# Kernel tuning notes

Measured on AMD Instinct MI355X. Metric: run time of the kernel, lower is better.

## Reference

```python
import jax, jax.numpy as jnp
import numpy as np

N_NODES = 50000
N_EDGES = 800000
N_LABEL_EDGES = 200000
IN_CH = 256
HID = 64
OUT_CH = 64


def gcn_conv(x, W, b, edge_index, n_nodes):
    """PyG GCNConv: symmetric-normalized aggregation with self-loops.
    out[col] = sum_row norm(row,col) * (x @ W)[row] + b
    """
    xw = x @ W  # [N, out]
    loops = jnp.arange(n_nodes, dtype=edge_index.dtype)
    row = jnp.concatenate([edge_index[0], loops])  # source
    col = jnp.concatenate([edge_index[1], loops])  # target
    deg = jax.ops.segment_sum(jnp.ones_like(col, dtype=xw.dtype), col, num_segments=n_nodes)
    dis = jnp.where(deg > 0, jax.lax.rsqrt(deg), 0.0)
    norm = dis[row] * dis[col]  # [E+N]
    out = jax.ops.segment_sum(xw[row] * norm[:, None], col, num_segments=n_nodes)
    return out + b


def setup_inputs() -> dict:
    key = jax.random.key(0)
    k0, k1, k2, k3, k4 = jax.random.split(key, 5)
    x = jax.random.normal(k0, (N_NODES, IN_CH), dtype=jnp.float32)
    edge_index = jax.random.randint(k1, (2, N_EDGES), 0, N_NODES, dtype=jnp.int32)
    edge_label_index = jax.random.randint(k2, (2, N_LABEL_EDGES), 0, N_NODES, dtype=jnp.int32)
    W1 = jax.random.normal(k3, (IN_CH, HID), dtype=jnp.float32) * (1.0 / np.sqrt(IN_CH))
    b1 = jnp.zeros((HID,), dtype=jnp.float32)
    W2 = jax.random.normal(k4, (HID, OUT_CH), dtype=jnp.float32) * (1.0 / np.sqrt(HID))
    b2 = jnp.zeros((OUT_CH,), dtype=jnp.float32)
    return {"x": x, "edge_index": edge_index, "edge_label_index": edge_label_index,
            "W1": W1, "b1": b1, "W2": W2, "b2": b2}


def reference(x, edge_index, edge_label_index, W1, b1, W2, b2):
    n = x.shape[0]
    # encode: two GCNConv layers with ReLU between
    h = jax.nn.relu(gcn_conv(x, W1, b1, edge_index, n))
    z = gcn_conv(h, W2, b2, edge_index, n)
    # decode: gather node pairs, elementwise multiply, sum over features
    src, dst = edge_label_index[0], edge_label_index[1]
    return jnp.sum(z[src] * z[dst], axis=1)  # [N_LABEL_EDGES]
```

## Files before the change

kernel.cpp:

```cpp
#include <hip/hip_runtime.h>
#include <hip/hip_bf16.h>


constexpr int NC = 256;
constexpr int NBPAD = 256;
constexpr int BSHIFT = 8;

__device__ __forceinline__ unsigned short f2bf(float f) {
    unsigned u = __float_as_uint(f);
    return (unsigned short)((u + 0x7FFF + ((u >> 16) & 1)) >> 16);
}
__device__ __forceinline__ float bf2f(unsigned short h) {
    return __uint_as_float(((unsigned)h) << 16);
}
__device__ __forceinline__ float4 bf4_to_f4(ushort4 u) {
    return make_float4(bf2f(u.x), bf2f(u.y), bf2f(u.z), bf2f(u.w));
}

__global__ __launch_bounds__(256) void hist_kernel(const int* __restrict__ col,
                                                   int* __restrict__ hist, int E, int CE) {
    __shared__ int hl[NBPAD];
    const int t = threadIdx.x, c = blockIdx.x;
    hl[t] = 0;
    __syncthreads();
    const int s = c * CE, e = min(E, s + CE);
    for (int i = s + t; i < e; i += 256) atomicAdd(&hl[col[i] >> BSHIFT], 1);
    __syncthreads();
    hist[t * NC + c] = hl[t];
}

__global__ __launch_bounds__(256) void bsum_kernel(const int* __restrict__ hist,
                                                   int* __restrict__ bsums) {
    __shared__ int red[256];
    const int t = threadIdx.x, b = blockIdx.x;
    red[t] = hist[b * NC + t];
    __syncthreads();
    for (int off = 128; off > 0; off >>= 1) {
        if (t < off) red[t] += red[t + off];
        __syncthreads();
    }
    if (t == 0) bsums[b] = red[0];
}

__global__ __launch_bounds__(256) void bscan_kernel(int* __restrict__ bsums) {
    __shared__ int sc[256];
    const int t = threadIdx.x;
    const int v = bsums[t];
    sc[t] = v;
    __syncthreads();
    for (int off = 1; off < 256; off <<= 1) {
        int u = (t >= off) ? sc[t - off] : 0;
        __syncthreads();
        sc[t] += u;
        __syncthreads();
    }
    bsums[t] = sc[t] - v;
}

__global__ __launch_bounds__(256) void rowscan_kernel(int* __restrict__ hist,
                                                      const int* __restrict__ bsums) {
    __shared__ int sc[256];
    const int t = threadIdx.x, b = blockIdx.x;
    const int v = hist[b * NC + t];
    sc[t] = v;
    __syncthreads();
    for (int off = 1; off < 256; off <<= 1) {
        int u = (t >= off) ? sc[t - off] : 0;
        __syncthreads();
        sc[t] += u;
        __syncthreads();
    }
    hist[b * NC + t] = sc[t] - v + bsums[b];
}

__global__ __launch_bounds__(256) void reorder_kernel(const int* __restrict__ row,
                                                      const int* __restrict__ col,
                                                      const int* __restrict__ hist,
                                                      int2* __restrict__ part, int E, int CE) {
    __shared__ int cur[NBPAD];
    const int t = threadIdx.x, c = blockIdx.x;
    cur[t] = hist[t * NC + c];
    __syncthreads();
    const int s = c * CE, e = min(E, s + CE);
    for (int i = s + t; i < e; i += 256) {
        const int r = row[i], cl = col[i];
        const int p = atomicAdd(&cur[cl >> BSHIFT], 1);
        part[p] = make_int2(r, cl);
    }
}

__global__ __launch_bounds__(256) void bucket_csr_kernel(const int2* __restrict__ part,
                                                         const int* __restrict__ hist,
                                                         int* __restrict__ csr,
                                                         int* __restrict__ offs,
                                                         float* __restrict__ dis,
                                                         int N, int E, int nbk) {
    __shared__ int cnt[256];
    __shared__ int sc[256];
    const int t = threadIdx.x, b = blockIdx.x;
    const int base = b << BSHIFT;
    const int bstart = hist[b * NC];
    const int bend = (b + 1 < NBPAD) ? hist[(b + 1) * NC] : E;
    const int m = bend - bstart;
    cnt[t] = 0;
    __syncthreads();
    for (int i = t; i < m; i += 256) atomicAdd(&cnt[part[bstart + i].y - base], 1);
    __syncthreads();
    const int v = cnt[t];
    sc[t] = v;
    __syncthreads();
    for (int off = 1; off < 256; off <<= 1) {
        int u = (t >= off) ? sc[t - off] : 0;
        __syncthreads();
        sc[t] += u;
        __syncthreads();
    }
    const int excl = sc[t] - v;
    const int node = base + t;
    if (node < N) {
        offs[node] = bstart + excl;
        dis[node] = rsqrtf((float)(v + 1));
    }
    sc[t] = excl;
    __syncthreads();
    for (int i = t; i < m; i += 256) {
        const int2 ec = part[bstart + i];
        const int p = atomicAdd(&sc[ec.y - base], 1);
        csr[bstart + p] = ec.x;
    }
    if (b == nbk - 1 && t == 0) offs[N] = E;
}

template <int K>
__global__ __launch_bounds__(256) void gemm_tile(const float* __restrict__ X,
                                                 const float* __restrict__ W,
                                                 const float* __restrict__ rowscale,
                                                 unsigned short* __restrict__ Y, int nrows) {
    __shared__ float sX[64 * 64];
    __shared__ float sW[64 * 64];
    const int tid = threadIdx.x;
    const int tx = tid & 15;
    const int ty = tid >> 4;
    const int rowbase = blockIdx.x * 64;

    float acc[16];
    #pragma unroll
    for (int i = 0; i < 16; ++i) acc[i] = 0.f;

    const int lr = tid & 63;
    const int lq = tid >> 6;
    int grow = rowbase + lr;
    if (grow >= nrows) grow = nrows - 1;
    const float* xrow = X + (long)grow * K;

    for (int kc = 0; kc < K; kc += 64) {
        if (kc) __syncthreads();
        #pragma unroll
        for (int i = 0; i < 4; ++i) {
            const int o = tid * 4 + i * 1024;
            *(float4*)&sW[o] = *(const float4*)&W[(long)kc * 64 + o];
        }
        #pragma unroll
        for (int t = 0; t < 4; ++t) {
            const int k = lq * 16 + t * 4;
            const float4 v = *(const float4*)&xrow[kc + k];
            sX[(k + 0) * 64 + lr] = v.x;
            sX[(k + 1) * 64 + lr] = v.y;
            sX[(k + 2) * 64 + lr] = v.z;
            sX[(k + 3) * 64 + lr] = v.w;
        }
        __syncthreads();
        #pragma unroll 4
        for (int k = 0; k < 64; ++k) {
            const float4 xv = *(const float4*)&sX[k * 64 + ty * 4];
            const float4 wv = *(const float4*)&sW[k * 64 + tx * 4];
            acc[0]  = fmaf(xv.x, wv.x, acc[0]);
            acc[1]  = fmaf(xv.x, wv.y, acc[1]);
            acc[2]  = fmaf(xv.x, wv.z, acc[2]);
            acc[3]  = fmaf(xv.x, wv.w, acc[3]);
            acc[4]  = fmaf(xv.y, wv.x, acc[4]);
            acc[5]  = fmaf(xv.y, wv.y, acc[5]);
            acc[6]  = fmaf(xv.y, wv.z, acc[6]);
            acc[7]  = fmaf(xv.y, wv.w, acc[7]);
            acc[8]  = fmaf(xv.z, wv.x, acc[8]);
            acc[9]  = fmaf(xv.z, wv.y, acc[9]);
            acc[10] = fmaf(xv.z, wv.z, acc[10]);
            acc[11] = fmaf(xv.z, wv.w, acc[11]);
            acc[12] = fmaf(xv.w, wv.x, acc[12]);
            acc[13] = fmaf(xv.w, wv.y, acc[13]);
            acc[14] = fmaf(xv.w, wv.z, acc[14]);
            acc[15] = fmaf(xv.w, wv.w, acc[15]);
        }
    }

    #pragma unroll
    for (int i = 0; i < 4; ++i) {
        const int orow = rowbase + ty * 4 + i;
        if (orow < nrows) {
            const float d = rowscale[orow];
            ushort4 ov;
            ov.x = f2bf(d * acc[i * 4 + 0]);
            ov.y = f2bf(d * acc[i * 4 + 1]);
            ov.z = f2bf(d * acc[i * 4 + 2]);
            ov.w = f2bf(d * acc[i * 4 + 3]);
            *(ushort4*)&Y[(long)orow * 64 + tx * 4] = ov;
        }
    }
}

template <bool RELU, bool OUT_BF16>
__global__ __launch_bounds__(256) void agg_kernel(const unsigned short* __restrict__ xs,
                                                  const int* __restrict__ csr,
                                                  const int* __restrict__ offs,
                                                  const float* __restrict__ dis,
                                                  const float* __restrict__ bias,
                                                  void* __restrict__ out, int n) {
    __shared__ int sidx[4][64];
    const int wv = threadIdx.x >> 6;
    const int lane = threadIdx.x & 63;
    const int grp = lane >> 4;
    const int fl = lane & 15;
    const int i = blockIdx.x * 4 + wv;
    if (i >= n) return;
    float4 acc = make_float4(0.f, 0.f, 0.f, 0.f);
    if (grp == 0)
        acc = bf4_to_f4(*(const ushort4*)&xs[(long)i * 64 + fl * 4]);
    const int s = offs[i];
    const int e = offs[i + 1];
    for (int jb = s; jb < e; jb += 64) {
        const int nb = min(64, e - jb);
        if (lane < nb) sidx[wv][lane] = csr[jb + lane];
        int u = grp;
        for (; u + 4 < nb; u += 8) {
            const int r0 = sidx[wv][u];
            const int r1 = sidx[wv][u + 4];
            const float4 v0 = bf4_to_f4(*(const ushort4*)&xs[(long)r0 * 64 + fl * 4]);
            const float4 v1 = bf4_to_f4(*(const ushort4*)&xs[(long)r1 * 64 + fl * 4]);
            acc.x += v0.x + v1.x; acc.y += v0.y + v1.y;
            acc.z += v0.z + v1.z; acc.w += v0.w + v1.w;
        }
        for (; u < nb; u += 4) {
            const int r0 = sidx[wv][u];
            const float4 v0 = bf4_to_f4(*(const ushort4*)&xs[(long)r0 * 64 + fl * 4]);
            acc.x += v0.x; acc.y += v0.y; acc.z += v0.z; acc.w += v0.w;
        }
    }
    acc.x += __shfl_xor(acc.x, 16); acc.y += __shfl_xor(acc.y, 16);
    acc.z += __shfl_xor(acc.z, 16); acc.w += __shfl_xor(acc.w, 16);
    acc.x += __shfl_xor(acc.x, 32); acc.y += __shfl_xor(acc.y, 32);
    acc.z += __shfl_xor(acc.z, 32); acc.w += __shfl_xor(acc.w, 32);
    if (grp == 0) {
        const float di = dis[i];
        const float4 b = *(const float4*)&bias[fl * 4];
        float4 o;
        o.x = fmaf(acc.x, di, b.x); o.y = fmaf(acc.y, di, b.y);
        o.z = fmaf(acc.z, di, b.z); o.w = fmaf(acc.w, di, b.w);
        if (RELU) {
            o.x = fmaxf(o.x, 0.f); o.y = fmaxf(o.y, 0.f);
            o.z = fmaxf(o.z, 0.f); o.w = fmaxf(o.w, 0.f);
        }
        if (OUT_BF16) {
            ushort4 ov;
            ov.x = f2bf(o.x); ov.y = f2bf(o.y); ov.z = f2bf(o.z); ov.w = f2bf(o.w);
            *(ushort4*)&((unsigned short*)out)[(long)i * 64 + fl * 4] = ov;
        } else {
            *(float4*)&((float*)out)[(long)i * 64 + fl * 4] = o;
        }
    }
}

__global__ __launch_bounds__(256) void decode_kernel(const unsigned short* __restrict__ z,
                                                     const int* __restrict__ src,
                                                     const int* __restrict__ dst,
                                                     float* __restrict__ out, int L) {
    const int t = blockIdx.x * 256 + threadIdx.x;
    const int e = t >> 4;
    const int fl = t & 15;
    if (e >= L) return;
    const int s = src[e];
    const int d = dst[e];
    const float4 a = bf4_to_f4(*(const ushort4*)&z[(long)s * 64 + fl * 4]);
    const float4 b = bf4_to_f4(*(const ushort4*)&z[(long)d * 64 + fl * 4]);
    float p = a.x * b.x + a.y * b.y + a.z * b.z + a.w * b.w;
    p += __shfl_xor(p, 8); p += __shfl_xor(p, 4);
    p += __shfl_xor(p, 2); p += __shfl_xor(p, 1);
    if (fl == 0) out[e] = p;
}

extern "C" void kernel_launch(void* const* d_in, const int* in_sizes, int n_in,
                              void* d_out, int out_size, void* d_ws, size_t ws_size,
                              hipStream_t stream) {
    const float* x   = (const float*)d_in[0];
    const int*   ei  = (const int*)d_in[1];
    const int*   eli = (const int*)d_in[2];
    const float* W1  = (const float*)d_in[3];
    const float* b1  = (const float*)d_in[4];
    const float* W2  = (const float*)d_in[5];
    const float* b2  = (const float*)d_in[6];
    float* out = (float*)d_out;

    const int N = in_sizes[0] / 256;
    const int E = in_sizes[1] / 2;
    const int L = in_sizes[2] / 2;
    const int* row = ei;
    const int* col = ei + E;
    const int* src = eli;
    const int* dst = eli + L;

    char* w = (char*)d_ws;
    unsigned short* xs = (unsigned short*)w;  w += (size_t)N * 64 * 2;
    float* h   = (float*)w;  w += (size_t)N * 64 * 4;
    unsigned short* z = (unsigned short*)w;  w += (size_t)N * 64 * 2;
    int*   csr = (int*)w;    w += (size_t)E * 4;
    int*   offs = (int*)w;   w += (size_t)(N + 1) * 4;
    float* dis = (float*)w;  w += (size_t)N * 4;
    int2*  part = (int2*)w;  w += (size_t)E * 8;
    int*  hist  = (int*)h;
    int*  bsums = hist + NBPAD * NC;

    const int CE = (E + NC - 1) / NC;
    const int nbk = (N + (1 << BSHIFT) - 1) >> BSHIFT;

    hist_kernel<<<NC, 256, 0, stream>>>(col, hist, E, CE);
    bsum_kernel<<<NBPAD, 256, 0, stream>>>(hist, bsums);
    bscan_kernel<<<1, 256, 0, stream>>>(bsums);
    rowscan_kernel<<<NBPAD, 256, 0, stream>>>(hist, bsums);
    reorder_kernel<<<NC, 256, 0, stream>>>(row, col, hist, part, E, CE);
    bucket_csr_kernel<<<nbk, 256, 0, stream>>>(part, hist, csr, offs, dis, N, E, nbk);

    gemm_tile<256><<<(N + 63) / 64, 256, 0, stream>>>(x, W1, dis, xs, N);
    agg_kernel<true, false><<<(N + 3) / 4, 256, 0, stream>>>(xs, csr, offs, dis, b1, h, N);
    gemm_tile<64><<<(N + 63) / 64, 256, 0, stream>>>(h, W2, dis, xs, N);
    agg_kernel<false, true><<<(N + 3) / 4, 256, 0, stream>>>(xs, csr, offs, dis, b2, z, N);
    decode_kernel<<<(L + 15) / 16, 256, 0, stream>>>(z, src, dst, out, L);
}
```

Before: 223.2 us.

## Widen gather loads to 16 bytes and fold histogram-sum/scan kernels into fewer launches

The aggregation and decode kernels now have each lane load 8 bf16 values (uint4) instead of 4. That halves the lanes per row and doubles the neighbor rows in flight per wave. The block-sum and block-scan kernels are removed: bucket totals are accumulated atomically in the histogram kernel, and every rowscan block rescans the 256 totals itself. The chunk count is doubled to 512, and rowscan now handles two entries per thread. This trades redundant scan work per block and extra global atomics for fewer launches and wider memory transactions.

```diff
diff --git a/kernel.cpp b/kernel.cpp
--- a/kernel.cpp
+++ b/kernel.cpp
@@ -2,7 +2,7 @@
 #include <hip/hip_bf16.h>
 
 
-constexpr int NC = 256;
+constexpr int NC = 512;
 constexpr int NBPAD = 256;
 constexpr int BSHIFT = 8;
 
@@ -10,15 +10,19 @@
     unsigned u = __float_as_uint(f);
     return (unsigned short)((u + 0x7FFF + ((u >> 16) & 1)) >> 16);
 }
-__device__ __forceinline__ float bf2f(unsigned short h) {
-    return __uint_as_float(((unsigned)h) << 16);
-}
-__device__ __forceinline__ float4 bf4_to_f4(ushort4 u) {
-    return make_float4(bf2f(u.x), bf2f(u.y), bf2f(u.z), bf2f(u.w));
+__device__ __forceinline__ float bflo(unsigned u) { return __uint_as_float(u << 16); }
+__device__ __forceinline__ float bfhi(unsigned u) { return __uint_as_float(u & 0xFFFF0000u); }
+
+__device__ __forceinline__ void bfacc8(float* acc, uint4 q) {
+    acc[0] += bflo(q.x); acc[1] += bfhi(q.x);
+    acc[2] += bflo(q.y); acc[3] += bfhi(q.y);
+    acc[4] += bflo(q.z); acc[5] += bfhi(q.z);
+    acc[6] += bflo(q.w); acc[7] += bfhi(q.w);
 }
 
 __global__ __launch_bounds__(256) void hist_kernel(const int* __restrict__ col,
-                                                   int* __restrict__ hist, int E, int CE) {
+                                                   int* __restrict__ hist,
+                                                   int* __restrict__ bsums, int E, int CE) {
     __shared__ int hl[NBPAD];
     const int t = threadIdx.x, c = blockIdx.x;
     hl[t] = 0;
@@ -26,27 +30,29 @@
     const int s = c * CE, e = min(E, s + CE);
     for (int i = s + t; i < e; i += 256) atomicAdd(&hl[col[i] >> BSHIFT], 1);
     __syncthreads();
-    hist[t * NC + c] = hl[t];
-}
-
-__global__ __launch_bounds__(256) void bsum_kernel(const int* __restrict__ hist,
-                                                   int* __restrict__ bsums) {
-    __shared__ int red[256];
+    const int v = hl[t];
+    hist[t * NC + c] = v;
+    if (v) atomicAdd(&bsums[t], v);
+}
+
+__global__ __launch_bounds__(256) void rowscan_kernel(int* __restrict__ hist,
+                                                      const int* __restrict__ bsums) {
+    __shared__ int sb[256];
+    __shared__ int sc[256];
     const int t = threadIdx.x, b = blockIdx.x;
-    red[t] = hist[b * NC + t];
-    __syncthreads();
-    for (int off = 128; off > 0; off >>= 1) {
-        if (t < off) red[t] += red[t + off];
-        __syncthreads();
-    }
-    if (t == 0) bsums[b] = red[0];
-}
-
-__global__ __launch_bounds__(256) void bscan_kernel(int* __restrict__ bsums) {
-    __shared__ int sc[256];
-    const int t = threadIdx.x;
-    const int v = bsums[t];
-    sc[t] = v;
+    sb[t] = bsums[t];
+    __syncthreads();
+    for (int off = 1; off < 256; off <<= 1) {
+        int u = (t >= off) ? sb[t - off] : 0;
+        __syncthreads();
+        sb[t] += u;
+        __syncthreads();
+    }
+    const int base = (b == 0) ? 0 : sb[b - 1];
+    const int i0 = b * NC + 2 * t;
+    const int a0 = hist[i0], a1 = hist[i0 + 1];
+    const int ps = a0 + a1;
+    sc[t] = ps;
     __syncthreads();
     for (int off = 1; off < 256; off <<= 1) {
         int u = (t >= off) ? sc[t - off] : 0;
@@ -54,23 +60,9 @@
         sc[t] += u;
         __syncthreads();
     }
-    bsums[t] = sc[t] - v;
-}
-
-__global__ __launch_bounds__(256) void rowscan_kernel(int* __restrict__ hist,
-                                                      const int* __restrict__ bsums) {
-    __shared__ int sc[256];
-    const int t = threadIdx.x, b = blockIdx.x;
-    const int v = hist[b * NC + t];
-    sc[t] = v;
-    __syncthreads();
-    for (int off = 1; off < 256; off <<= 1) {
-        int u = (t >= off) ? sc[t - off] : 0;
-        __syncthreads();
-        sc[t] += u;
-        __syncthreads();
-    }
-    hist[b * NC + t] = sc[t] - v + bsums[b];
+    const int excl = sc[t] - ps;
+    hist[i0] = base + excl;
+    hist[i0 + 1] = base + excl + a0;
 }
 
 __global__ __launch_bounds__(256) void reorder_kernel(const int* __restrict__ row,
@@ -218,53 +210,64 @@
     __shared__ int sidx[4][64];
     const int wv = threadIdx.x >> 6;
     const int lane = threadIdx.x & 63;
-    const int grp = lane >> 4;
-    const int fl = lane & 15;
+    const int grp = lane >> 3;
+    const int fl = lane & 7;
     const int i = blockIdx.x * 4 + wv;
     if (i >= n) return;
-    float4 acc = make_float4(0.f, 0.f, 0.f, 0.f);
+    float acc[8];
+    #pragma unroll
+    for (int j = 0; j < 8; ++j) acc[j] = 0.f;
     if (grp == 0)
-        acc = bf4_to_f4(*(const ushort4*)&xs[(long)i * 64 + fl * 4]);
+        bfacc8(acc, *(const uint4*)&xs[(long)i * 64 + fl * 8]);
     const int s = offs[i];
     const int e = offs[i + 1];
     for (int jb = s; jb < e; jb += 64) {
         const int nb = min(64, e - jb);
         if (lane < nb) sidx[wv][lane] = csr[jb + lane];
         int u = grp;
-        for (; u + 4 < nb; u += 8) {
+        for (; u + 8 < nb; u += 16) {
             const int r0 = sidx[wv][u];
-            const int r1 = sidx[wv][u + 4];
-            const float4 v0 = bf4_to_f4(*(const ushort4*)&xs[(long)r0 * 64 + fl * 4]);
-            const float4 v1 = bf4_to_f4(*(const ushort4*)&xs[(long)r1 * 64 + fl * 4]);
-            acc.x += v0.x + v1.x; acc.y += v0.y + v1.y;
-            acc.z += v0.z + v1.z; acc.w += v0.w + v1.w;
-        }
-        for (; u < nb; u += 4) {
+            const int r1 = sidx[wv][u + 8];
+            const uint4 q0 = *(const uint4*)&xs[(long)r0 * 64 + fl * 8];
+            const uint4 q1 = *(const uint4*)&xs[(long)r1 * 64 + fl * 8];
+            bfacc8(acc, q0);
+            bfacc8(acc, q1);
+        }
+        for (; u < nb; u += 8) {
             const int r0 = sidx[wv][u];
-            const float4 v0 = bf4_to_f4(*(const ushort4*)&xs[(long)r0 * 64 + fl * 4]);
-            acc.x += v0.x; acc.y += v0.y; acc.z += v0.z; acc.w += v0.w;
-        }
-    }
-    acc.x += __shfl_xor(acc.x, 16); acc.y += __shfl_xor(acc.y, 16);
-    acc.z += __shfl_xor(acc.z, 16); acc.w += __shfl_xor(acc.w, 16);
-    acc.x += __shfl_xor(acc.x, 32); acc.y += __shfl_xor(acc.y, 32);
-    acc.z += __shfl_xor(acc.z, 32); acc.w += __shfl_xor(acc.w, 32);
+            bfacc8(acc, *(const uint4*)&xs[(long)r0 * 64 + fl * 8]);
+        }
+    }
+    #pragma unroll
+    for (int j = 0; j < 8; ++j) {
+        acc[j] += __shfl_xor(acc[j], 8);
+        acc[j] += __shfl_xor(acc[j], 16);
+        acc[j] += __shfl_xor(acc[j], 32);
+    }
     if (grp == 0) {
         const float di = dis[i];
-        const float4 b = *(const float4*)&bias[fl * 4];
-        float4 o;
-        o.x = fmaf(acc.x, di, b.x); o.y = fmaf(acc.y, di, b.y);
-        o.z = fmaf(acc.z, di, b.z); o.w = fmaf(acc.w, di, b.w);
+        const float4 b0 = *(const float4*)&bias[fl * 8 + 0];
+        const float4 b4 = *(const float4*)&bias[fl * 8 + 4];
+        float o[8];
+        o[0] = fmaf(acc[0], di, b0.x); o[1] = fmaf(acc[1], di, b0.y);
+        o[2] = fmaf(acc[2], di, b0.z); o[3] = fmaf(acc[3], di, b0.w);
+        o[4] = fmaf(acc[4], di, b4.x); o[5] = fmaf(acc[5], di, b4.y);
+        o[6] = fmaf(acc[6], di, b4.z); o[7] = fmaf(acc[7], di, b4.w);
         if (RELU) {
-            o.x = fmaxf(o.x, 0.f); o.y = fmaxf(o.y, 0.f);
-            o.z = fmaxf(o.z, 0.f); o.w = fmaxf(o.w, 0.f);
+            #pragma unroll
+            for (int j = 0; j < 8; ++j) o[j] = fmaxf(o[j], 0.f);
         }
         if (OUT_BF16) {
-            ushort4 ov;
-            ov.x = f2bf(o.x); ov.y = f2bf(o.y); ov.z = f2bf(o.z); ov.w = f2bf(o.w);
-            *(ushort4*)&((unsigned short*)out)[(long)i * 64 + fl * 4] = ov;
+            uint4 q;
+            q.x = (unsigned)f2bf(o[0]) | ((unsigned)f2bf(o[1]) << 16);
+            q.y = (unsigned)f2bf(o[2]) | ((unsigned)f2bf(o[3]) << 16);
+            q.z = (unsigned)f2bf(o[4]) | ((unsigned)f2bf(o[5]) << 16);
+            q.w = (unsigned)f2bf(o[6]) | ((unsigned)f2bf(o[7]) << 16);
+            *(uint4*)&((unsigned short*)out)[(long)i * 64 + fl * 8] = q;
         } else {
-            *(float4*)&((float*)out)[(long)i * 64 + fl * 4] = o;
+            float* op = (float*)out + (long)i * 64 + fl * 8;
+            *(float4*)&op[0] = make_float4(o[0], o[1], o[2], o[3]);
+            *(float4*)&op[4] = make_float4(o[4], o[5], o[6], o[7]);
         }
     }
 }
@@ -274,16 +277,18 @@
                                                      const int* __restrict__ dst,
                                                      float* __restrict__ out, int L) {
     const int t = blockIdx.x * 256 + threadIdx.x;
-    const int e = t >> 4;
-    const int fl = t & 15;
+    const int e = t >> 3;
+    const int fl = t & 7;
     if (e >= L) return;
     const int s = src[e];
     const int d = dst[e];
-    const float4 a = bf4_to_f4(*(const ushort4*)&z[(long)s * 64 + fl * 4]);
-    const float4 b = bf4_to_f4(*(const ushort4*)&z[(long)d * 64 + fl * 4]);
-    float p = a.x * b.x + a.y * b.y + a.z * b.z + a.w * b.w;
-    p += __shfl_xor(p, 8); p += __shfl_xor(p, 4);
-    p += __shfl_xor(p, 2); p += __shfl_xor(p, 1);
+    const uint4 qa = *(const uint4*)&z[(long)s * 64 + fl * 8];
+    const uint4 qb = *(const uint4*)&z[(long)d * 64 + fl * 8];
+    float p = bflo(qa.x) * bflo(qb.x) + bfhi(qa.x) * bfhi(qb.x)
+            + bflo(qa.y) * bflo(qb.y) + bfhi(qa.y) * bfhi(qb.y)
+            + bflo(qa.z) * bflo(qb.z) + bfhi(qa.z) * bfhi(qb.z)
+            + bflo(qa.w) * bflo(qb.w) + bfhi(qa.w) * bfhi(qb.w);
+    p += __shfl_xor(p, 4); p += __shfl_xor(p, 2); p += __shfl_xor(p, 1);
     if (fl == 0) out[e] = p;
 }
 
@@ -321,9 +326,8 @@
     const int CE = (E + NC - 1) / NC;
     const int nbk = (N + (1 << BSHIFT) - 1) >> BSHIFT;
 
-    hist_kernel<<<NC, 256, 0, stream>>>(col, hist, E, CE);
-    bsum_kernel<<<NBPAD, 256, 0, stream>>>(hist, bsums);
-    bscan_kernel<<<1, 256, 0, stream>>>(bsums);
+    hipMemsetAsync(bsums, 0, NBPAD * sizeof(int), stream);
+    hist_kernel<<<NC, 256, 0, stream>>>(col, hist, bsums, E, CE);
     rowscan_kernel<<<NBPAD, 256, 0, stream>>>(hist, bsums);
     reorder_kernel<<<NC, 256, 0, stream>>>(row, col, hist, part, E, CE);
     bucket_csr_kernel<<<nbk, 256, 0, stream>>>(part, hist, csr, offs, dis, N, E, nbk);
@@ -332,5 +336,5 @@
     agg_kernel<true, false><<<(N + 3) / 4, 256, 0, stream>>>(xs, csr, offs, dis, b1, h, N);
     gemm_tile<64><<<(N + 63) / 64, 256, 0, stream>>>(h, W2, dis, xs, N);
     agg_kernel<false, true><<<(N + 3) / 4, 256, 0, stream>>>(xs, csr, offs, dis, b2, z, N);
-    decode_kernel<<<(L + 15) / 16, 256, 0, stream>>>(z, src, dst, out, L);
-}
+    decode_kernel<<<(L * 8 + 255) / 256, 256, 0, stream>>>(z, src, dst, out, L);
+}
```

Result: slower. 228.2 us (+2.2%).
